# Optimization experiments

Measured on AMD Instinct MI355X. Metric: run time of the kernel, lower is better.

The kernel has to match this reference:

```python
import jax, jax.numpy as jnp
import numpy as np

NEG = -1e30  # safe -inf surrogate for log-space DP
BLANK = 0    # torch.nn.CTCLoss default blank index


def _ctc_loss_sum(lp, labels, in_lens, lab_lens):
    """CTC negative log-likelihood, summed over batch.
    lp: [T, B, V] log-probabilities; labels: [B, L] int; in_lens, lab_lens: [B] int.
    """
    T, B, V = lp.shape
    L = labels.shape[1]
    S = 2 * L + 1  # extended label length (blanks interleaved)
    s = jnp.arange(S)
    # extended label sequence z: blank at even positions, label at odd
    ext = jnp.where(s % 2 == 0, BLANK, labels[:, jnp.clip((s - 1) // 2, 0, L - 1)])  # [B,S]
    ext_m2 = jnp.concatenate([jnp.full((B, 2), BLANK, ext.dtype), ext[:, :-2]], axis=1)
    skip = (s >= 2) & (ext != BLANK) & (ext != ext_m2)  # [B,S] skip-transition allowed
    # emission log-probs gathered at extended labels: [T,B,S]
    emit = jnp.take_along_axis(lp, jnp.broadcast_to(ext[None], (T, B, S)), axis=2)
    alpha0 = jnp.full((B, S), NEG, lp.dtype)
    alpha0 = alpha0.at[:, 0].set(emit[0, :, 0]).at[:, 1].set(emit[0, :, 1])

    def step(alpha, inputs):
        emit_t, t = inputs
        a1 = jnp.concatenate([jnp.full((B, 1), NEG, alpha.dtype), alpha[:, :-1]], axis=1)
        a2 = jnp.concatenate([jnp.full((B, 2), NEG, alpha.dtype), alpha[:, :-2]], axis=1)
        comb = jnp.logaddexp(alpha, a1)
        comb = jnp.where(skip, jnp.logaddexp(comb, a2), comb)
        new = comb + emit_t
        # past each sequence's length, freeze alpha
        new = jnp.where(t < in_lens[:, None], new, alpha)
        return new, None

    alpha, _ = jax.lax.scan(step, alpha0, (emit[1:], jnp.arange(1, T)))
    s_last = 2 * lab_lens  # final blank position per sample
    bidx = jnp.arange(B)
    ll = jnp.logaddexp(alpha[bidx, s_last], alpha[bidx, s_last - 1])
    return jnp.sum(-ll)


def setup_inputs() -> dict:
    key = jax.random.key(0)
    k1, k2, k3, k4, k5, k6 = jax.random.split(key, 6)
    B, T, H, V, L = 16, 512, 512, 4096, 64
    hs_pad = jax.random.normal(k1, (B, T, H), dtype=jnp.float32)
    hs_lens = jax.random.randint(k2, (B,), T // 2, T + 1, dtype=jnp.int32)
    ys_pad = jax.random.randint(k3, (B, L), 1, V, dtype=jnp.int32)  # avoid blank=0
    ys_lens = jax.random.randint(k4, (B,), L // 2, L + 1, dtype=jnp.int32)
    W = jax.random.normal(k5, (H, V), dtype=jnp.float32) * (H ** -0.5)
    b = jax.random.normal(k6, (V,), dtype=jnp.float32) * 0.01
    return {"hs_pad": hs_pad, "hs_lens": hs_lens, "ys_pad": ys_pad,
            "ys_lens": ys_lens, "W": W, "b": b}


def reference(hs_pad, hs_lens, ys_pad, ys_lens, W, b):
    # projection (dropout_rate=0.0 -> identity) + log_softmax
    logits = jnp.einsum('bth,hv->btv', hs_pad, W) + b
    log_probs = jax.nn.log_softmax(logits, axis=-1)
    lp = jnp.transpose(log_probs, (1, 0, 2))  # [T,B,V]
    B = lp.shape[1]
    loss = _ctc_loss_sum(lp, ys_pad, hs_lens, ys_lens)
    return loss / B
```

## Files before the change

### kernel.cpp

```cpp
#include <hip/hip_runtime.h>
#include <hip/hip_bf16.h>
#include <math.h>

#define BB   16
#define TT   512
#define HH   512
#define VV   4096
#define LL   64
#define SS   129
#define JJ   65
#define MM   (BB*TT)

#define LOG2E 1.4426950408889634f
#define LN2   0.6931471805599453f

typedef __bf16 bf16;
typedef __attribute__((ext_vector_type(4))) __bf16 bf16x4;
typedef __attribute__((ext_vector_type(8))) __bf16 bf16x8;
typedef __attribute__((ext_vector_type(4))) float f32x4;

__global__ __launch_bounds__(256) void prep(const float* __restrict__ hs,
                                            const float* __restrict__ W,
                                            bf16* __restrict__ Abf,
                                            bf16* __restrict__ Wt)
{
    __shared__ float t[64][65];
    const int tid = threadIdx.x;
    int bx = blockIdx.x;
    if (bx < 4096) {
        int idx = bx * 256 + tid;
        float4 v = ((const float4*)hs)[idx];
        bf16x4 o = {(bf16)v.x, (bf16)v.y, (bf16)v.z, (bf16)v.w};
        *(bf16x4*)(Abf + (size_t)idx * 4) = o;
    } else {
        bx -= 4096;
        const int n0 = (bx & 63) * 64;
        const int k0 = (bx >> 6) * 64;
        #pragma unroll
        for (int i = 0; i < 16; ++i) {
            int idx = tid + i * 256;
            int kk = idx >> 6, nn = idx & 63;
            t[kk][nn] = W[(size_t)(k0 + kk) * VV + n0 + nn];
        }
        __syncthreads();
        #pragma unroll
        for (int i = 0; i < 16; ++i) {
            int idx = tid + i * 256;
            int nl = idx >> 6, kk = idx & 63;
            Wt[(size_t)(n0 + nl) * HH + k0 + kk] = (bf16)t[kk][nl];
        }
    }
}

#define TN 128
#define NT64 (VV / 64)

#define GLDS(src, dst) \
    __builtin_amdgcn_global_load_lds((const __attribute__((address_space(1))) void*)(src), \
                                     (__attribute__((address_space(3))) void*)(dst), 16, 0, 0)

__global__ __launch_bounds__(256) void gemm_lse_mfma(
    const bf16* __restrict__ A,
    const bf16* __restrict__ Bt,
    const float* __restrict__ bias,
    const int*  __restrict__ ys,
    float* __restrict__ part,
    float* __restrict__ glpT)
{
    __shared__ bf16 As[128 * 32];
    __shared__ bf16 Bs[128 * 32];
    const int tid = threadIdx.x;
    const int lane = tid & 63;
    const int wid = tid >> 6;
    const int wm = wid >> 1, wn = wid & 1;
    const int m0 = blockIdx.y * 128, n0 = blockIdx.x * 128;
    const int lq = lane & 15, kg = lane >> 4;

    f32x4 acc[4][4];
    const f32x4 z = {0.f, 0.f, 0.f, 0.f};
    #pragma unroll
    for (int i = 0; i < 4; ++i)
        #pragma unroll
        for (int j = 0; j < 4; ++j) acc[i][j] = z;

    const int c0 = tid;
    const int row0 = c0 >> 2, sl0 = (c0 & 3) ^ (row0 & 3);
    const int c1 = tid + 256;
    const int row1 = c1 >> 2, sl1 = (c1 & 3) ^ (row1 & 3);
    bf16* dstA0 = As + (size_t)(0 * 256 + (tid & 192)) * 8;
    bf16* dstA1 = As + (size_t)(1 * 256 + (tid & 192)) * 8;
    bf16* dstB0 = Bs + (size_t)(0 * 256 + (tid & 192)) * 8;
    bf16* dstB1 = Bs + (size_t)(1 * 256 + (tid & 192)) * 8;
    const bf16* srcA0 = A  + (size_t)(m0 + row0) * HH + sl0 * 8;
    const bf16* srcA1 = A  + (size_t)(m0 + row1) * HH + sl1 * 8;
    const bf16* srcB0 = Bt + (size_t)(n0 + row0) * HH + sl0 * 8;
    const bf16* srcB1 = Bt + (size_t)(n0 + row1) * HH + sl1 * 8;

    for (int k0 = 0; k0 < HH; k0 += 32) {
        GLDS(srcA0 + k0, dstA0);
        GLDS(srcA1 + k0, dstA1);
        GLDS(srcB0 + k0, dstB0);
        GLDS(srcB1 + k0, dstB1);
        __syncthreads();
        bf16x8 a[4], b[4];
        #pragma unroll
        for (int i = 0; i < 4; ++i) {
            int ar = wm * 64 + i * 16 + lq;
            a[i] = *(const bf16x8*)&As[ar * 32 + ((kg ^ (ar & 3)) * 8)];
        }
        #pragma unroll
        for (int j = 0; j < 4; ++j) {
            int br = wn * 64 + j * 16 + lq;
            b[j] = *(const bf16x8*)&Bs[br * 32 + ((kg ^ (br & 3)) * 8)];
        }
        #pragma unroll
        for (int i = 0; i < 4; ++i)
            #pragma unroll
            for (int j = 0; j < 4; ++j)
                acc[i][j] = __builtin_amdgcn_mfma_f32_16x16x32_bf16(a[i], b[j], acc[i][j], 0, 0, 0);
        __syncthreads();
    }

    const int ct = blockIdx.x * 2 + wn;
    float bj[4];
    #pragma unroll
    for (int j = 0; j < 4; ++j) bj[j] = bias[n0 + wn * 64 + j * 16 + lq];
    #pragma unroll
    for (int i = 0; i < 4; ++i) {
        #pragma unroll
        for (int r = 0; r < 4; ++r) {
            float v[4], mx = -3.4e38f;
            #pragma unroll
            for (int j = 0; j < 4; ++j) { v[j] = acc[i][j][r] + bj[j]; mx = fmaxf(mx, v[j]); }
            #pragma unroll
            for (int d = 1; d < 16; d <<= 1) mx = fmaxf(mx, __shfl_xor(mx, d));
            float sm = 0.f;
            #pragma unroll
            for (int j = 0; j < 4; ++j) sm += __expf(v[j] - mx);
            #pragma unroll
            for (int d = 1; d < 16; d <<= 1) sm += __shfl_xor(sm, d);
            if (lq == 0) {
                int rowg = m0 + wm * 64 + i * 16 + kg * 4 + r;
                size_t o = ((size_t)rowg * NT64 + ct) * 2;
                part[o] = mx; part[o + 1] = sm;
            }
        }
    }

    const int bidx = m0 >> 9;
    const int t0s  = (m0 & 511) + wm * 64;
    const int nbase = n0 + wn * 64;
    for (int j = 0; j < JJ; ++j) {
        int c = (j == 0) ? 0 : ys[bidx * LL + j - 1];
        int local = c - nbase;
        if (local >= 0 && local < 64) {
            int cl = local & 15;
            float bc = bias[c];
            #pragma unroll
            for (int jt = 0; jt < 4; ++jt) {
                if ((local >> 4) == jt && lq == cl) {
                    float* dst = glpT + ((size_t)(bidx * JJ + j)) * TT + t0s + kg * 4;
                    #pragma unroll
                    for (int i = 0; i < 4; ++i) {
                        f32x4 sv = acc[i][jt];
                        float4 o4 = {sv[0] + bc, sv[1] + bc, sv[2] + bc, sv[3] + bc};
                        *(float4*)(dst + i * 16) = o4;
                    }
                }
            }
        }
    }
}

__global__ __launch_bounds__(256) void lse_merge(const float* __restrict__ part,
                                                 float* __restrict__ lse)
{
    const int lane = threadIdx.x & 63;
    const int r = blockIdx.x * 4 + (threadIdx.x >> 6);
    const float* p = part + (size_t)r * (NT64 * 2);
    float mx = p[2 * lane];
    float sm = p[2 * lane + 1];
    float wmax = mx;
    #pragma unroll
    for (int d = 1; d < 64; d <<= 1) wmax = fmaxf(wmax, __shfl_xor(wmax, d));
    float c = sm * __expf(mx - wmax);
    #pragma unroll
    for (int d = 1; d < 64; d <<= 1) c += __shfl_xor(c, d);
    if (lane == 0) lse[r] = wmax + logf(c);
}

__device__ __forceinline__ float dpp_shr1_zero(float x) {
    int r = __builtin_amdgcn_update_dpp(0, __float_as_int(x),
                                        0x138 , 0xF, 0xF, false);
    return __int_as_float(r);
}
template<int CTRL>
__device__ __forceinline__ float dpp_max_t(float m) {
    int r = __builtin_amdgcn_update_dpp(0, __float_as_int(m), CTRL, 0xF, 0xF, false);
    return fmaxf(m, __int_as_float(r));
}

#define LOADA(rv, gv, blk) { \
    int bb_ = (blk); bb_ = bb_ < 32 ? bb_ : 31; \
    const float4* p0_ = (const float4*)(g0 + bb_ * 16); \
    const float4* pB_ = (const float4*)(gB + bb_ * 16); \
    float4 q0_[4], qB_[4]; \
    q0_[0] = p0_[0]; q0_[1] = p0_[1]; q0_[2] = p0_[2]; q0_[3] = p0_[3]; \
    qB_[0] = pB_[0]; qB_[1] = pB_[1]; qB_[2] = pB_[2]; qB_[3] = pB_[3]; \
    _Pragma("unroll") \
    for (int u = 0; u < 16; ++u) { \
        float raw0_ = ((const float*)q0_)[u]; \
        float rawB_ = ((const float*)qB_)[u]; \
        rv[u] = __builtin_amdgcn_exp2f((rawB_ - raw0_) * LOG2E); \
        gv[u] = raw0_; \
    } }

#define RESCALE() { \
        float m_ = fmaxf(fmaxf(vA ? A : 0.f, vB ? B : 0.f), vC ? C : 0.f); \
        m_ = dpp_max_t<0x111>(m_);  \
        m_ = dpp_max_t<0x112>(m_);  \
        m_ = dpp_max_t<0x114>(m_);  \
        m_ = dpp_max_t<0x118>(m_);  \
        m_ = dpp_max_t<0x142>(m_);  \
        m_ = dpp_max_t<0x143>(m_);  \
        int mb = __builtin_amdgcn_readlane(__float_as_int(m_), 63); \
        int k_ = ((mb >> 23) & 0xFF) - 127; \
        float sc = __int_as_float((127 - k_) << 23); \
        A *= sc; B *= sc; C *= sc; K += k_; \
    }

#define DO16(rv, gv, blk, SKIP0) { \
    const int tB_ = (blk) * 16; \
    if (!(SKIP0) && tB_ + 16 <= Tin) { \
        _Pragma("unroll") \
        for (int u = 0; u < 16; ++u) { \
            float prevB = dpp_shr1_zero(B); \
            float nA = A + prevB; \
            float t1 = A + B; \
            float t2 = skipB ? prevB : 0.f; \
            float nB = (t1 + t2) * rv[u]; \
            float nC = C + B; \
            A = nA; B = nB; C = nC; corr += gv[u]; \
            if (u == 7 || u == 15) RESCALE(); \
        } \
    } else { \
        _Pragma("unroll") \
        for (int u = 0; u < 16; ++u) { \
            int t_ = tB_ + u; \
            bool upd = (t_ >= 1) && (t_ < Tin); \
            float prevB = dpp_shr1_zero(B); \
            float nA = A + prevB; \
            float t1 = A + B; \
            float t2 = skipB ? prevB : 0.f; \
            float nB = (t1 + t2) * rv[u]; \
            float nC = C + B; \
            A = upd ? nA : A; B = upd ? nB : B; C = upd ? nC : C; \
            corr += upd ? gv[u] : 0.f; \
            if (u == 7 || u == 15) RESCALE(); \
        } \
    } }

__global__ __launch_bounds__(64) void ctc_dp(
    const float* __restrict__ glpT, const float* __restrict__ lse,
    const int* __restrict__ ys, const int* __restrict__ hs_lens,
    const int* __restrict__ ys_lens, float* __restrict__ nll)
{
    const int b = blockIdx.x;
    const int l = threadIdx.x;
    const float* g0 = glpT + (size_t)(b * JJ) * TT;
    const float* gB = glpT + (size_t)(b * JJ + l + 1) * TT;
    const float* ls = lse + (size_t)b * TT;
    const int Tin = hs_lens[b];
    const int Ll  = ys_lens[b];

    const bool vA = (l <= Ll);
    const bool vB = (l <  Ll);
    const bool vC = (l == 63) && (Ll == 64);

    int cc = ys[b * LL + l];
    bool skipB = false;
    if (l >= 1) { int cp = ys[b * LL + l - 1]; skipB = (cc != 0) && (cc != cp); }

    float raw0_0 = g0[0];
    float d0 = (gB[0] - raw0_0) * LOG2E;
    float A = (l == 0) ? 1.0f : 0.0f;
    float B = (l == 0) ? __builtin_amdgcn_exp2f(d0) : 0.0f;
    float C = 0.0f;
    float corr = raw0_0;
    int K = 0;

    float ra[16], ga[16], rb[16], gb[16];
    LOADA(ra, ga, 0);
    for (int blk = 0; blk < 32; blk += 2) {
        LOADA(rb, gb, blk + 1);
        DO16(ra, ga, blk, (blk == 0));
        LOADA(ra, ga, blk + 2);
        DO16(rb, gb, blk + 1, false);
        if (16 * (blk + 2) >= Tin) break;
    }

    float lsum = 0.f;
    for (int tt = l; tt < Tin; tt += 64) lsum += ls[tt];
    #pragma unroll
    for (int d = 1; d < 64; d <<= 1) lsum += __shfl_xor(lsum, d);

    float v1 = (Ll == 64) ? __shfl(C, 63, 64) : __shfl(A, Ll, 64);
    float v2 = __shfl(B, Ll - 1, 64);
    if (l == 0) {
        float ll2 = __builtin_amdgcn_logf(v1 + v2) + (float)K + (corr - lsum) * LOG2E;
        nll[b] = -ll2 * LN2;
    }
}

__global__ void finalize(const float* __restrict__ nll, float* __restrict__ out)
{
    float v = (threadIdx.x < BB) ? nll[threadIdx.x] : 0.f;
    #pragma unroll
    for (int d = 32; d >= 1; d >>= 1) v += __shfl_down(v, d);
    if (threadIdx.x == 0) out[0] = v / (float)BB;
}

extern "C" void kernel_launch(void* const* d_in, const int* in_sizes, int n_in,
                              void* d_out, int out_size, void* d_ws, size_t ws_size,
                              hipStream_t stream) {
    const float* hs      = (const float*)d_in[0];
    const int*   hs_lens = (const int*)  d_in[1];
    const int*   ys      = (const int*)  d_in[2];
    const int*   ys_lens = (const int*)  d_in[3];
    const float* W       = (const float*)d_in[4];
    const float* bias    = (const float*)d_in[5];
    float* out = (float*)d_out;

    float* ws   = (float*)d_ws;
    float* part = ws;
    float* lse  = part + (size_t)MM * NT64 * 2;
    float* glpT = lse  + MM;
    float* nll  = glpT + (size_t)BB * JJ * TT;
    bf16*  Abf  = (bf16*)(nll + 16);
    bf16*  Wt   = Abf + (size_t)MM * HH;

    prep<<<4608, 256, 0, stream>>>(hs, W, Abf, Wt);
    gemm_lse_mfma<<<dim3(VV / TN, MM / 128), 256, 0, stream>>>(Abf, Wt, bias, ys, part, glpT);
    lse_merge<<<MM / 4, 256, 0, stream>>>(part, lse);
    ctc_dp<<<BB, 64, 0, stream>>>(glpT, lse, ys, hs_lens, ys_lens, nll);
    finalize<<<1, 64, 0, stream>>>(nll, out);
}
```

Measured before the change: 199.8 us.

## Deepen CTC DP load prefetch, batch corr sums, use DPP row reductions

In the CTC DP kernel, raw float4 loads are now issued two blocks ahead, and the exp2 ratio plus the correction sum are computed just before each block. This moves the serial corr accumulation off the critical recurrence chain and overlaps global memory latency better. In the GEMM epilogue, the 16-lane shuffle reductions are replaced with DPP row reductions. The vectorized float4 emission store is split into scalar stores. The extra prefetch stage adds register pressure.

```diff
diff --git a/kernel.cpp b/kernel.cpp
--- a/kernel.cpp
+++ b/kernel.cpp
@@ -18,6 +18,36 @@
 typedef __attribute__((ext_vector_type(4))) __bf16 bf16x4;
 typedef __attribute__((ext_vector_type(8))) __bf16 bf16x8;
 typedef __attribute__((ext_vector_type(4))) float f32x4;
+
+template<int CTRL>
+__device__ __forceinline__ float dpp_mov(float x) {
+    return __int_as_float(__builtin_amdgcn_update_dpp(
+        __float_as_int(x), __float_as_int(x), CTRL, 0xF, 0xF, false));
+}
+__device__ __forceinline__ float row16_max(float x) {
+    x = fmaxf(x, dpp_mov<0x128>(x));
+    x = fmaxf(x, dpp_mov<0x124>(x));
+    x = fmaxf(x, dpp_mov<0x122>(x));
+    x = fmaxf(x, dpp_mov<0x121>(x));
+    return x;
+}
+__device__ __forceinline__ float row16_sum(float x) {
+    x += dpp_mov<0x128>(x);
+    x += dpp_mov<0x124>(x);
+    x += dpp_mov<0x122>(x);
+    x += dpp_mov<0x121>(x);
+    return x;
+}
+__device__ __forceinline__ float dpp_shr1_zero(float x) {
+    int r = __builtin_amdgcn_update_dpp(0, __float_as_int(x),
+                                        0x138 , 0xF, 0xF, false);
+    return __int_as_float(r);
+}
+template<int CTRL>
+__device__ __forceinline__ float dpp_max_t(float m) {
+    int r = __builtin_amdgcn_update_dpp(0, __float_as_int(m), CTRL, 0xF, 0xF, false);
+    return fmaxf(m, __int_as_float(r));
+}
 
 __global__ __launch_bounds__(256) void prep(const float* __restrict__ hs,
                                             const float* __restrict__ W,
@@ -132,13 +162,11 @@
             float v[4], mx = -3.4e38f;
             #pragma unroll
             for (int j = 0; j < 4; ++j) { v[j] = acc[i][j][r] + bj[j]; mx = fmaxf(mx, v[j]); }
-            #pragma unroll
-            for (int d = 1; d < 16; d <<= 1) mx = fmaxf(mx, __shfl_xor(mx, d));
+            mx = row16_max(mx);
             float sm = 0.f;
             #pragma unroll
             for (int j = 0; j < 4; ++j) sm += __expf(v[j] - mx);
-            #pragma unroll
-            for (int d = 1; d < 16; d <<= 1) sm += __shfl_xor(sm, d);
+            sm = row16_sum(sm);
             if (lq == 0) {
                 int rowg = m0 + wm * 64 + i * 16 + kg * 4 + r;
                 size_t o = ((size_t)rowg * NT64 + ct) * 2;
@@ -159,13 +187,13 @@
             #pragma unroll
             for (int jt = 0; jt < 4; ++jt) {
                 if ((local >> 4) == jt && lq == cl) {
-                    float* dst = glpT + ((size_t)(bidx * JJ + j)) * TT + t0s + kg * 4;
                     #pragma unroll
-                    for (int i = 0; i < 4; ++i) {
-                        f32x4 sv = acc[i][jt];
-                        float4 o4 = {sv[0] + bc, sv[1] + bc, sv[2] + bc, sv[3] + bc};
-                        *(float4*)(dst + i * 16) = o4;
-                    }
+                    for (int i = 0; i < 4; ++i)
+                        #pragma unroll
+                        for (int r = 0; r < 4; ++r) {
+                            int tt = t0s + i * 16 + kg * 4 + r;
+                            glpT[(size_t)(bidx * JJ + j) * TT + tt] = acc[i][jt][r] + bc;
+                        }
                 }
             }
         }
@@ -189,30 +217,37 @@
     if (lane == 0) lse[r] = wmax + logf(c);
 }
 
-__device__ __forceinline__ float dpp_shr1_zero(float x) {
-    int r = __builtin_amdgcn_update_dpp(0, __float_as_int(x),
-                                        0x138 , 0xF, 0xF, false);
-    return __int_as_float(r);
-}
-template<int CTRL>
-__device__ __forceinline__ float dpp_max_t(float m) {
-    int r = __builtin_amdgcn_update_dpp(0, __float_as_int(m), CTRL, 0xF, 0xF, false);
-    return fmaxf(m, __int_as_float(r));
-}
-
-#define LOADA(rv, gv, blk) { \
+#define F4AT(arr, u) ( ((u) & 3) == 0 ? arr[(u) >> 2].x \
+                     : ((u) & 3) == 1 ? arr[(u) >> 2].y \
+                     : ((u) & 3) == 2 ? arr[(u) >> 2].z : arr[(u) >> 2].w )
+
+#define LOADI(p0v, pBv, blk) { \
     int bb_ = (blk); bb_ = bb_ < 32 ? bb_ : 31; \
     const float4* p0_ = (const float4*)(g0 + bb_ * 16); \
     const float4* pB_ = (const float4*)(gB + bb_ * 16); \
-    float4 q0_[4], qB_[4]; \
-    q0_[0] = p0_[0]; q0_[1] = p0_[1]; q0_[2] = p0_[2]; q0_[3] = p0_[3]; \
-    qB_[0] = pB_[0]; qB_[1] = pB_[1]; qB_[2] = pB_[2]; qB_[3] = pB_[3]; \
+    p0v[0] = p0_[0]; p0v[1] = p0_[1]; p0v[2] = p0_[2]; p0v[3] = p0_[3]; \
+    pBv[0] = pB_[0]; pBv[1] = pB_[1]; pBv[2] = pB_[2]; pBv[3] = pB_[3]; \
+}
+
+#define RVCOMP(rv, p0v, pBv, blk) { \
+    const int tB_ = (blk) * 16; \
     _Pragma("unroll") \
     for (int u = 0; u < 16; ++u) { \
-        float raw0_ = ((const float*)q0_)[u]; \
-        float rawB_ = ((const float*)qB_)[u]; \
-        rv[u] = __builtin_amdgcn_exp2f((rawB_ - raw0_) * LOG2E); \
-        gv[u] = raw0_; \
+        rv[u] = __builtin_amdgcn_exp2f((F4AT(pBv, u) - F4AT(p0v, u)) * LOG2E); \
+    } \
+    if (tB_ > 0 && tB_ + 16 <= Tin) { \
+        float s_ = 0.f; \
+        _Pragma("unroll") \
+        for (int u = 0; u < 16; ++u) s_ += F4AT(p0v, u); \
+        corr += s_; \
+    } else { \
+        float s_ = 0.f; \
+        _Pragma("unroll") \
+        for (int u = 0; u < 16; ++u) { \
+            int t_ = tB_ + u; \
+            s_ += (t_ >= 1 && t_ < Tin) ? F4AT(p0v, u) : 0.f; \
+        } \
+        corr += s_; \
     } }
 
 #define RESCALE() { \
@@ -229,9 +264,9 @@
         A *= sc; B *= sc; C *= sc; K += k_; \
     }
 
-#define DO16(rv, gv, blk, SKIP0) { \
+#define DO16N(rv, blk) { \
     const int tB_ = (blk) * 16; \
-    if (!(SKIP0) && tB_ + 16 <= Tin) { \
+    if (tB_ > 0 && tB_ + 16 <= Tin) { \
         _Pragma("unroll") \
         for (int u = 0; u < 16; ++u) { \
             float prevB = dpp_shr1_zero(B); \
@@ -240,7 +275,7 @@
             float t2 = skipB ? prevB : 0.f; \
             float nB = (t1 + t2) * rv[u]; \
             float nC = C + B; \
-            A = nA; B = nB; C = nC; corr += gv[u]; \
+            A = nA; B = nB; C = nC; \
             if (u == 7 || u == 15) RESCALE(); \
         } \
     } else { \
@@ -255,7 +290,6 @@
             float nB = (t1 + t2) * rv[u]; \
             float nC = C + B; \
             A = upd ? nA : A; B = upd ? nB : B; C = upd ? nC : C; \
-            corr += upd ? gv[u] : 0.f; \
             if (u == 7 || u == 15) RESCALE(); \
         } \
     } }
@@ -289,13 +323,17 @@
     float corr = raw0_0;
     int K = 0;
 
-    float ra[16], ga[16], rb[16], gb[16];
-    LOADA(ra, ga, 0);
+    float4 p0a[4], pBa[4], p0b[4], pBb[4];
+    float rva[16], rvb[16];
+    LOADI(p0a, pBa, 0);
+    LOADI(p0b, pBb, 1);
     for (int blk = 0; blk < 32; blk += 2) {
-        LOADA(rb, gb, blk + 1);
-        DO16(ra, ga, blk, (blk == 0));
-        LOADA(ra, ga, blk + 2);
-        DO16(rb, gb, blk + 1, false);
+        RVCOMP(rva, p0a, pBa, blk);
+        LOADI(p0a, pBa, blk + 2);
+        DO16N(rva, blk);
+        RVCOMP(rvb, p0b, pBb, blk + 1);
+        LOADI(p0b, pBb, blk + 3);
+        DO16N(rvb, blk + 1);
         if (16 * (blk + 2) >= Tin) break;
     }
 
```

New measurement: 187.3 us. 6.3% less time.
